# Kernel optimization log

Measured on AMD Instinct MI355X. Metric: run time of the kernel, lower is better.

Reference implementation:

```python
import jax, jax.numpy as jnp
import numpy as np

USER_NUM = 100000
ITEM_NUM = 50000
N_NODES = USER_NUM + ITEM_NUM
EMB_DIM = 64
N_LAYERS = 3
NNZ = 4800000


def setup_inputs() -> dict:
    key = jax.random.key(0)
    k1, k2, k3, k4, k5 = jax.random.split(key, 5)
    user_emb = 0.2 * jax.random.normal(k1, (USER_NUM, EMB_DIM), dtype=jnp.float32)
    item_emb = 0.2 * jax.random.normal(k2, (ITEM_NUM, EMB_DIM), dtype=jnp.float32)
    adj_row = jax.random.randint(k3, (NNZ,), 0, N_NODES, dtype=jnp.int32)
    adj_col = jax.random.randint(k4, (NNZ,), 0, N_NODES, dtype=jnp.int32)
    adj_vals = jax.random.uniform(k5, (NNZ,), dtype=jnp.float32)
    return {
        "user_emb": user_emb,
        "item_emb": item_emb,
        "adj_row": adj_row,
        "adj_col": adj_col,
        "adj_vals": adj_vals,
    }


def _spmm(row, col, vals, x):
    # sparse [N,N] @ dense [N,D] via gather + weighted segment-sum
    msg = vals[:, None] * x[col]  # [nnz, D]
    return jax.ops.segment_sum(msg, row, num_segments=N_NODES)


def reference(user_emb, item_emb, adj_row, adj_col, adj_vals):
    ego = jnp.concatenate([user_emb, item_emb], axis=0)  # [N, D]
    acc = ego  # running sum over layers (equivalent to stack+mean)
    for _ in range(N_LAYERS):
        ego = _spmm(adj_row, adj_col, adj_vals, ego)
        acc = acc + ego
    out = acc / jnp.asarray(N_LAYERS + 1, dtype=acc.dtype)
    return out[:USER_NUM], out[USER_NUM:]
```

## Files before the change

### kernel.cpp

```cpp
#include <hip/hip_runtime.h>

#define USER_NUM 100000
#define ITEM_NUM 50000
#define N_NODES  150000
#define EMB_DIM  64
#define NNZ      4800000

#define CB_SHIFT 10
#define ROWS_PER_CB 1024
#define NCB ((N_NODES + ROWS_PER_CB - 1) / ROWS_PER_CB)
#define CB_CAP 34000
#define TILE 4096
#define NTILES ((NNZ + TILE - 1) / TILE)
#define EPT 16

__device__ __forceinline__ float bflo(unsigned u) {
    return __uint_as_float(u << 16);
}
__device__ __forceinline__ float bfhi(unsigned u) {
    return __uint_as_float(u & 0xFFFF0000u);
}
__device__ __forceinline__ unsigned f2bf(float f) {
    unsigned u = __float_as_uint(f);
    return (u + 0x7FFFu + ((u >> 16) & 1u)) >> 16;
}

__global__ void lgcn_init(const float4* __restrict__ user,
                          const float4* __restrict__ item,
                          uint4* __restrict__ xb) {
    int i = blockIdx.x * blockDim.x + threadIdx.x;
    if (i >= N_NODES * 8) return;
    const int user_chunks = USER_NUM * 8;
    float4 f0, f1;
    if (i < user_chunks) {
        f0 = user[i * 2];
        f1 = user[i * 2 + 1];
    } else {
        f0 = item[(i - user_chunks) * 2];
        f1 = item[(i - user_chunks) * 2 + 1];
    }
    uint4 p;
    p.x = f2bf(f0.x) | (f2bf(f0.y) << 16);
    p.y = f2bf(f0.z) | (f2bf(f0.w) << 16);
    p.z = f2bf(f1.x) | (f2bf(f1.y) << 16);
    p.w = f2bf(f1.z) | (f2bf(f1.w) << 16);
    xb[i] = p;
}

__global__ void lgcn_bcur_init(int* __restrict__ bucket_cursor) {
    int b = blockIdx.x * blockDim.x + threadIdx.x;
    if (b < NCB) bucket_cursor[b] = b * CB_CAP;
}

__global__ __launch_bounds__(256) void lgcn_partition(
    const int* __restrict__ row,
    const int* __restrict__ col,
    const float* __restrict__ vals,
    int* __restrict__ bucket_cursor,
    int2* __restrict__ t_cv) {
    __shared__ int hist[NCB];
    __shared__ int excl[NCB];
    __shared__ int delta[NCB];
    __shared__ unsigned meta[TILE];
    __shared__ int cols[TILE];
    __shared__ float vls[TILE];
    __shared__ int sscan[256];

    int tid = threadIdx.x;
    int tileStart = blockIdx.x * TILE;
    int tileCount = NNZ - tileStart;
    if (tileCount > TILE) tileCount = TILE;

    for (int b = tid; b < NCB; b += 256) hist[b] = 0;
    __syncthreads();

    int rws[EPT];
#pragma unroll
    for (int k = 0; k < EPT; ++k) {
        int le = tid + k * 256;
        int r = -1;
        if (le < tileCount) {
            r = row[tileStart + le];
            atomicAdd(&hist[r >> CB_SHIFT], 1);
        }
        rws[k] = r;
    }
    __syncthreads();

    int h = (tid < NCB) ? hist[tid] : 0;
    sscan[tid] = h;
    __syncthreads();
    for (int off = 1; off < 256; off <<= 1) {
        int x = (tid >= off) ? sscan[tid - off] : 0;
        __syncthreads();
        sscan[tid] += x;
        __syncthreads();
    }
    if (tid < NCB) {
        int ex = sscan[tid] - h;
        excl[tid] = ex;
        int rb = h ? atomicAdd(&bucket_cursor[tid], h) : 0;
        delta[tid] = rb - ex;
    }
    __syncthreads();

#pragma unroll
    for (int k = 0; k < EPT; ++k) {
        int le = tid + k * 256;
        if (le < tileCount) {
            int e = tileStart + le;
            int cc = col[e];
            float vv = vals[e];
            int r = rws[k];
            int b = r >> CB_SHIFT;
            int lp = atomicAdd(&excl[b], 1);
            meta[lp] = ((unsigned)b << 10) | (unsigned)(r & (ROWS_PER_CB - 1));
            cols[lp] = cc;
            vls[lp] = vv;
        }
    }
    __syncthreads();

    for (int i = tid; i < tileCount; i += 256) {
        unsigned m = meta[i];
        int b = m >> 10;
        int rlo = m & (ROWS_PER_CB - 1);
        int gpos = delta[b] + i;
        if (gpos < (b + 1) * CB_CAP) {
            t_cv[gpos] = make_int2((rlo << 18) | cols[i],
                                   __float_as_int(vls[i]));
        }
    }
}

__global__ __launch_bounds__(1024) void lgcn_finalize(
    const int* __restrict__ bucket_cursor,
    const int2* __restrict__ t_cv,
    int2* __restrict__ csr_cv,
    int2* __restrict__ row_se) {
    __shared__ int hist[ROWS_PER_CB];
    __shared__ int cur[ROWS_PER_CB];
    __shared__ int sscan[1024];
    int t = threadIdx.x;
    int b = blockIdx.x;

    int v = 0;
    if (t < NCB) {
        int cb = bucket_cursor[t] - t * CB_CAP;
        v = (cb > CB_CAP) ? CB_CAP : cb;
    }
    if (t < 256) sscan[t] = v;
    __syncthreads();
    for (int off = 1; off < 256; off <<= 1) {
        int x = 0;
        if (t < 256 && t >= off) x = sscan[t - off];
        __syncthreads();
        if (t < 256) sscan[t] += x;
        __syncthreads();
    }
    int prev = (b == 0) ? 0 : sscan[b - 1];
    int bbase = prev;
    int count = sscan[b] - prev;
    __syncthreads();

    int lo = b * ROWS_PER_CB;
    int nrows = N_NODES - lo;
    if (nrows > ROWS_PER_CB) nrows = ROWS_PER_CB;

    hist[t] = 0;
    __syncthreads();

    int base = b * CB_CAP;
    int eEnd = base + count;
    int e = base + t;
    for (; e + 3 * 1024 < eEnd; e += 4 * 1024) {
        int2 c0 = t_cv[e];
        int2 c1 = t_cv[e + 1024];
        int2 c2 = t_cv[e + 2048];
        int2 c3 = t_cv[e + 3072];
        atomicAdd(&hist[(unsigned)c0.x >> 18], 1);
        atomicAdd(&hist[(unsigned)c1.x >> 18], 1);
        atomicAdd(&hist[(unsigned)c2.x >> 18], 1);
        atomicAdd(&hist[(unsigned)c3.x >> 18], 1);
    }
    for (; e < eEnd; e += 1024)
        atomicAdd(&hist[(unsigned)t_cv[e].x >> 18], 1);
    __syncthreads();

    int h = hist[t];
    sscan[t] = h;
    __syncthreads();
    for (int off = 1; off < 1024; off <<= 1) {
        int x = (t >= off) ? sscan[t - off] : 0;
        __syncthreads();
        sscan[t] += x;
        __syncthreads();
    }
    int p = bbase + sscan[t] - h;
    if (t < nrows) {
        row_se[lo + t] = make_int2(p, p + h);
        cur[t] = p;
    }
    __syncthreads();

    e = base + t;
    for (; e + 3 * 1024 < eEnd; e += 4 * 1024) {
        int2 c0 = t_cv[e];
        int2 c1 = t_cv[e + 1024];
        int2 c2 = t_cv[e + 2048];
        int2 c3 = t_cv[e + 3072];
        int p0 = atomicAdd(&cur[(unsigned)c0.x >> 18], 1);
        int p1 = atomicAdd(&cur[(unsigned)c1.x >> 18], 1);
        int p2 = atomicAdd(&cur[(unsigned)c2.x >> 18], 1);
        int p3 = atomicAdd(&cur[(unsigned)c3.x >> 18], 1);
        csr_cv[p0] = make_int2(c0.x & 0x3FFFF, c0.y);
        csr_cv[p1] = make_int2(c1.x & 0x3FFFF, c1.y);
        csr_cv[p2] = make_int2(c2.x & 0x3FFFF, c2.y);
        csr_cv[p3] = make_int2(c3.x & 0x3FFFF, c3.y);
    }
    for (; e < eEnd; e += 1024) {
        int2 cv = t_cv[e];
        int pos = atomicAdd(&cur[(unsigned)cv.x >> 18], 1);
        csr_cv[pos] = make_int2(cv.x & 0x3FFFF, cv.y);
    }
}

#define FMA8(vv, uu) do {                                          \
    a[0] += (vv) * bflo((uu).x); a[1] += (vv) * bfhi((uu).x);      \
    a[2] += (vv) * bflo((uu).y); a[3] += (vv) * bfhi((uu).y);      \
    a[4] += (vv) * bflo((uu).z); a[5] += (vv) * bfhi((uu).z);      \
    a[6] += (vv) * bflo((uu).w); a[7] += (vv) * bfhi((uu).w);      \
} while (0)

#define SPMM_BODY                                                  \
    int gid = blockIdx.x * blockDim.x + threadIdx.x;               \
    int r = gid >> 6;                                              \
    if (r >= N_NODES) return;                                      \
    int lane = threadIdx.x & 63;                                   \
    int c = lane & 7;                                              \
    int sub = lane >> 3;                                           \
    int2 se = row_se[r];                                           \
    int start = se.x;                                              \
    int end = se.y;                                                \
    float a[8] = {0.f, 0.f, 0.f, 0.f, 0.f, 0.f, 0.f, 0.f};         \
    int e = start + sub;                                           \
    for (; e + 24 < end; e += 32) {                                \
        int2 cv0 = csr_cv[e];                                      \
        int2 cv1 = csr_cv[e + 8];                                  \
        int2 cv2 = csr_cv[e + 16];                                 \
        int2 cv3 = csr_cv[e + 24];                                 \
        uint4 u0 = xb[cv0.x * 8 + c];                              \
        uint4 u1 = xb[cv1.x * 8 + c];                              \
        uint4 u2 = xb[cv2.x * 8 + c];                              \
        uint4 u3 = xb[cv3.x * 8 + c];                              \
        float v0 = __int_as_float(cv0.y);                          \
        float v1 = __int_as_float(cv1.y);                          \
        float v2 = __int_as_float(cv2.y);                          \
        float v3 = __int_as_float(cv3.y);                          \
        FMA8(v0, u0);                                              \
        FMA8(v1, u1);                                              \
        FMA8(v2, u2);                                              \
        FMA8(v3, u3);                                              \
    }                                                              \
    if (e + 8 < end) {                                             \
        int2 cv0 = csr_cv[e];                                      \
        int2 cv1 = csr_cv[e + 8];                                  \
        uint4 u0 = xb[cv0.x * 8 + c];                              \
        uint4 u1 = xb[cv1.x * 8 + c];                              \
        float v0 = __int_as_float(cv0.y);                          \
        float v1 = __int_as_float(cv1.y);                          \
        FMA8(v0, u0);                                              \
        FMA8(v1, u1);                                              \
        e += 16;                                                   \
    }                                                              \
    if (e < end) {                                                 \
        int2 cv = csr_cv[e];                                       \
        uint4 u = xb[cv.x * 8 + c];                                \
        float v = __int_as_float(cv.y);                            \
        FMA8(v, u);                                                \
    }                                                              \
    _Pragma("unroll")                                              \
    for (int k = 0; k < 8; ++k) {                                  \
        a[k] += __shfl_xor(a[k], 8);                               \
        a[k] += __shfl_xor(a[k], 16);                              \
        a[k] += __shfl_xor(a[k], 32);                              \
    }

__global__ __launch_bounds__(256, 8) void lgcn_spmm_bf16(
    const int2* __restrict__ row_se,
    const int2* __restrict__ csr_cv,
    const uint4* __restrict__ xb,
    uint4* __restrict__ yb) {
    SPMM_BODY
    if (sub == 0) {
        uint4 p;
        p.x = f2bf(a[0]) | (f2bf(a[1]) << 16);
        p.y = f2bf(a[2]) | (f2bf(a[3]) << 16);
        p.z = f2bf(a[4]) | (f2bf(a[5]) << 16);
        p.w = f2bf(a[6]) | (f2bf(a[7]) << 16);
        yb[r * 8 + c] = p;
    }
}

__global__ __launch_bounds__(256, 8) void lgcn_spmm_final(
    const int2* __restrict__ row_se,
    const int2* __restrict__ csr_cv,
    const uint4* __restrict__ xb,
    const uint4* __restrict__ x0b,
    const uint4* __restrict__ y1b,
    float4* __restrict__ out) {
    SPMM_BODY
    if (sub == 0) {
        uint4 q0 = x0b[r * 8 + c];
        uint4 q1 = y1b[r * 8 + c];
        uint4 q2 = xb[r * 8 + c];
        float4 o0, o1;
        o0.x = (bflo(q0.x) + bflo(q1.x) + bflo(q2.x) + a[0]) * 0.25f;
        o0.y = (bfhi(q0.x) + bfhi(q1.x) + bfhi(q2.x) + a[1]) * 0.25f;
        o0.z = (bflo(q0.y) + bflo(q1.y) + bflo(q2.y) + a[2]) * 0.25f;
        o0.w = (bfhi(q0.y) + bfhi(q1.y) + bfhi(q2.y) + a[3]) * 0.25f;
        o1.x = (bflo(q0.z) + bflo(q1.z) + bflo(q2.z) + a[4]) * 0.25f;
        o1.y = (bfhi(q0.z) + bfhi(q1.z) + bfhi(q2.z) + a[5]) * 0.25f;
        o1.z = (bflo(q0.w) + bflo(q1.w) + bflo(q2.w) + a[6]) * 0.25f;
        o1.w = (bfhi(q0.w) + bfhi(q1.w) + bfhi(q2.w) + a[7]) * 0.25f;
        int idx = r * 16 + c * 2;
        out[idx] = o0;
        out[idx + 1] = o1;
    }
}

extern "C" void kernel_launch(void* const* d_in, const int* in_sizes, int n_in,
                              void* d_out, int out_size, void* d_ws, size_t ws_size,
                              hipStream_t stream) {
    const float* user_emb = (const float*)d_in[0];
    const float* item_emb = (const float*)d_in[1];
    const int*   adj_row  = (const int*)d_in[2];
    const int*   adj_col  = (const int*)d_in[3];
    const float* adj_vals = (const float*)d_in[4];
    float* out = (float*)d_out;

    char* base = (char*)d_ws;
    uint4* xb_a   = (uint4*)base;
    int2*  csr_cv = (int2*)(base + 19200000);
    char*  S      = base + 57600000;
    const size_t T_ENTRIES = (size_t)NCB * CB_CAP;
    int2*  t_cv   = (int2*)S;
    uint4* y1b    = (uint4*)S;
    uint4* y2b    = (uint4*)(S + 19200000);
    char*  tail   = S + T_ENTRIES * 8;
    int2*  row_se = (int2*)tail;
    int*   bucket_cursor = (int*)(tail + (size_t)N_NODES * 8);

    {
        int threads = 256;
        int blocks = (N_NODES * 8 + threads - 1) / threads;
        lgcn_init<<<blocks, threads, 0, stream>>>(
            (const float4*)user_emb, (const float4*)item_emb, xb_a);
    }

    lgcn_bcur_init<<<1, 256, 0, stream>>>(bucket_cursor);
    lgcn_partition<<<NTILES, 256, 0, stream>>>(
        adj_row, adj_col, adj_vals, bucket_cursor, t_cv);
    lgcn_finalize<<<NCB, 1024, 0, stream>>>(
        bucket_cursor, t_cv, csr_cv, row_se);

    const int spmm_block = 256;
    const int spmm_grid = (N_NODES * 64 + spmm_block - 1) / spmm_block;
    lgcn_spmm_bf16<<<spmm_grid, spmm_block, 0, stream>>>(
        row_se, csr_cv, xb_a, y1b);
    lgcn_spmm_bf16<<<spmm_grid, spmm_block, 0, stream>>>(
        row_se, csr_cv, y1b, y2b);
    lgcn_spmm_final<<<spmm_grid, spmm_block, 0, stream>>>(
        row_se, csr_cv, y2b, xb_a, y1b, (float4*)out);
}
```

Before: 505.8 us.

## Streamline partition: reuse histogram atomics as slots, pad cursors, fuse cursor init

```diff
diff --git a/kernel.cpp b/kernel.cpp
--- a/kernel.cpp
+++ b/kernel.cpp
@@ -10,9 +10,10 @@
 #define ROWS_PER_CB 1024
 #define NCB ((N_NODES + ROWS_PER_CB - 1) / ROWS_PER_CB)
 #define CB_CAP 34000
-#define TILE 4096
+#define TILE 8192
 #define NTILES ((NNZ + TILE - 1) / TILE)
-#define EPT 16
+#define EPT 32
+#define CUR_STRIDE 16
 
 __device__ __forceinline__ float bflo(unsigned u) {
     return __uint_as_float(u << 16);
@@ -27,8 +28,10 @@
 
 __global__ void lgcn_init(const float4* __restrict__ user,
                           const float4* __restrict__ item,
-                          uint4* __restrict__ xb) {
+                          uint4* __restrict__ xb,
+                          int* __restrict__ bucket_cursor) {
     int i = blockIdx.x * blockDim.x + threadIdx.x;
+    if (i < NCB) bucket_cursor[i * CUR_STRIDE] = i * CB_CAP;
     if (i >= N_NODES * 8) return;
     const int user_chunks = USER_NUM * 8;
     float4 f0, f1;
@@ -47,23 +50,16 @@
     xb[i] = p;
 }
 
-__global__ void lgcn_bcur_init(int* __restrict__ bucket_cursor) {
-    int b = blockIdx.x * blockDim.x + threadIdx.x;
-    if (b < NCB) bucket_cursor[b] = b * CB_CAP;
-}
-
 __global__ __launch_bounds__(256) void lgcn_partition(
     const int* __restrict__ row,
     const int* __restrict__ col,
     const float* __restrict__ vals,
     int* __restrict__ bucket_cursor,
     int2* __restrict__ t_cv) {
-    __shared__ int hist[NCB];
-    __shared__ int excl[NCB];
+    __shared__ int histB[NCB];
     __shared__ int delta[NCB];
-    __shared__ unsigned meta[TILE];
-    __shared__ int cols[TILE];
-    __shared__ float vls[TILE];
+    __shared__ int2 pcv[TILE];
+    __shared__ unsigned char bb[TILE];
     __shared__ int sscan[256];
 
     int tid = threadIdx.x;
@@ -71,23 +67,25 @@
     int tileCount = NNZ - tileStart;
     if (tileCount > TILE) tileCount = TILE;
 
-    for (int b = tid; b < NCB; b += 256) hist[b] = 0;
+    for (int b = tid; b < NCB; b += 256) histB[b] = 0;
     __syncthreads();
 
     int rws[EPT];
+    int lps[EPT];
 #pragma unroll
     for (int k = 0; k < EPT; ++k) {
         int le = tid + k * 256;
-        int r = -1;
+        int r = -1, lp = 0;
         if (le < tileCount) {
             r = row[tileStart + le];
-            atomicAdd(&hist[r >> CB_SHIFT], 1);
+            lp = atomicAdd(&histB[r >> CB_SHIFT], 1);
         }
         rws[k] = r;
-    }
-    __syncthreads();
-
-    int h = (tid < NCB) ? hist[tid] : 0;
+        lps[k] = lp;
+    }
+    __syncthreads();
+
+    int h = (tid < NCB) ? histB[tid] : 0;
     sscan[tid] = h;
     __syncthreads();
     for (int off = 1; off < 256; off <<= 1) {
@@ -96,11 +94,12 @@
         sscan[tid] += x;
         __syncthreads();
     }
+    __syncthreads();
     if (tid < NCB) {
-        int ex = sscan[tid] - h;
-        excl[tid] = ex;
-        int rb = h ? atomicAdd(&bucket_cursor[tid], h) : 0;
-        delta[tid] = rb - ex;
+        int sb = sscan[tid] - h;
+        histB[tid] = sb;
+        int rb = h ? atomicAdd(&bucket_cursor[tid * CUR_STRIDE], h) : 0;
+        delta[tid] = rb - sb;
     }
     __syncthreads();
 
@@ -113,23 +112,19 @@
             float vv = vals[e];
             int r = rws[k];
             int b = r >> CB_SHIFT;
-            int lp = atomicAdd(&excl[b], 1);
-            meta[lp] = ((unsigned)b << 10) | (unsigned)(r & (ROWS_PER_CB - 1));
-            cols[lp] = cc;
-            vls[lp] = vv;
+            int slot = histB[b] + lps[k];
+            pcv[slot] = make_int2(((r & (ROWS_PER_CB - 1)) << 18) | cc,
+                                  __float_as_int(vv));
+            bb[slot] = (unsigned char)b;
         }
     }
     __syncthreads();
 
     for (int i = tid; i < tileCount; i += 256) {
-        unsigned m = meta[i];
-        int b = m >> 10;
-        int rlo = m & (ROWS_PER_CB - 1);
+        int b = bb[i];
         int gpos = delta[b] + i;
-        if (gpos < (b + 1) * CB_CAP) {
-            t_cv[gpos] = make_int2((rlo << 18) | cols[i],
-                                   __float_as_int(vls[i]));
-        }
+        if (gpos < (b + 1) * CB_CAP)
+            t_cv[gpos] = pcv[i];
     }
 }
 
@@ -146,7 +141,7 @@
 
     int v = 0;
     if (t < NCB) {
-        int cb = bucket_cursor[t] - t * CB_CAP;
+        int cb = bucket_cursor[t * CUR_STRIDE] - t * CB_CAP;
         v = (cb > CB_CAP) ? CB_CAP : cb;
     }
     if (t < 256) sscan[t] = v;
@@ -355,10 +350,10 @@
         int threads = 256;
         int blocks = (N_NODES * 8 + threads - 1) / threads;
         lgcn_init<<<blocks, threads, 0, stream>>>(
-            (const float4*)user_emb, (const float4*)item_emb, xb_a);
-    }
-
-    lgcn_bcur_init<<<1, 256, 0, stream>>>(bucket_cursor);
+            (const float4*)user_emb, (const float4*)item_emb, xb_a,
+            bucket_cursor);
+    }
+
     lgcn_partition<<<NTILES, 256, 0, stream>>>(
         adj_row, adj_col, adj_vals, bucket_cursor, t_cv);
     lgcn_finalize<<<NCB, 1024, 0, stream>>>(
```

After: 520.4 us. 1.03x slower.
